# Kernel optimization log

Hardware: AMD Instinct MI355X
Metric: run time of the kernel (lower is better)

## Reference

```python
import jax, jax.numpy as jnp
import numpy as np

D_MODEL = 1024
NUM_HEADS = 16
HEAD_DIM = D_MODEL // NUM_HEADS


def setup_inputs() -> dict:
    key = jax.random.key(0)
    ks = jax.random.split(key, 5)
    x = jax.random.normal(ks[0], (4, 2048, D_MODEL), dtype=jnp.float32)
    # xavier_uniform with gain=0.1 for square (D,D) weights: limit = 0.1*sqrt(6/(D+D))
    limit = 0.1 * np.sqrt(6.0 / (2 * D_MODEL))
    def w(k):
        return jax.random.uniform(k, (D_MODEL, D_MODEL), jnp.float32, -limit, limit)
    return {
        "x": x,
        "W_q": w(ks[1]), "b_q": jnp.zeros((D_MODEL,), jnp.float32),
        "W_k": w(ks[2]), "b_k": jnp.zeros((D_MODEL,), jnp.float32),
        "W_v": w(ks[3]), "b_v": jnp.zeros((D_MODEL,), jnp.float32),
        "W_o": w(ks[4]), "b_o": jnp.zeros((D_MODEL,), jnp.float32),
    }


def reference(x, W_q, b_q, W_k, b_k, W_v, b_v, W_o, b_o):
    B, S, D = x.shape
    H, Hd = NUM_HEADS, HEAD_DIM
    # Linear: x @ W^T + b (torch nn.Linear convention); weights here are (out, in)
    def proj(W, b):
        y = jnp.einsum('bsd,ed->bse', x, W) + b
        return y.reshape(B, S, H, Hd).transpose(0, 2, 1, 3)  # [B,H,S,Hd]
    Q = proj(W_q, b_q)
    K = proj(W_k, b_k)
    V = proj(W_v, b_v)
    scale = 1.0 / np.sqrt(Hd).astype(np.float32)
    scores = jnp.einsum('bhqd,bhkd->bhqk', Q, K) * scale  # [B,H,S,S]
    attn = jax.nn.softmax(scores, axis=-1)
    ctx = jnp.einsum('bhqk,bhkd->bhqd', attn, V)
    ctx = ctx.transpose(0, 2, 1, 3).reshape(B, S, D)
    out = jnp.einsum('bsd,ed->bse', ctx, W_o) + b_o
    return out
```

## Files before the change

### kernel.cpp

```cpp
#include <hip/hip_runtime.h>
#include <math.h>

#define B_  4
#define S_  2048
#define D_  1024
#define H_  16
#define HD_ 64
#define M_  (B_*S_)

typedef short short8 __attribute__((ext_vector_type(8)));
typedef float f32x4 __attribute__((ext_vector_type(4)));

#define MFMA16(a,b,c) __builtin_amdgcn_mfma_f32_16x16x32_bf16(a, b, c, 0, 0, 0)

#if __has_builtin(__builtin_amdgcn_exp2f)
#define EXP2(x) __builtin_amdgcn_exp2f(x)
#else
#define EXP2(x) exp2f(x)
#endif

__device__ __forceinline__ unsigned short f2bf(float f) {
    unsigned u = __float_as_uint(f);
    u = (u + 0x7FFF + ((u >> 16) & 1)) >> 16;
    return (unsigned short)u;
}

__device__ __forceinline__ unsigned pack_bf16(float a, float b) {
#if __has_builtin(__builtin_amdgcn_cvt_pk_bf16_f32)
    typedef __bf16 bf2 __attribute__((ext_vector_type(2)));
    bf2 v = __builtin_amdgcn_cvt_pk_bf16_f32(a, b);
    unsigned r;
    __builtin_memcpy(&r, &v, 4);
    return r;
#else
    unsigned ua = __float_as_uint(a), ub = __float_as_uint(b);
    ua += 0x7FFFu + ((ua >> 16) & 1u);
    ub += 0x7FFFu + ((ub >> 16) & 1u);
    return __builtin_amdgcn_perm(ub, ua, 0x07060302u);
#endif
}

__device__ __forceinline__ void async_copy16(const void* g, void* l) {
    __builtin_amdgcn_global_load_lds(
        (const __attribute__((address_space(1))) void*)g,
        (__attribute__((address_space(3))) void*)l, 16, 0, 0);
}

__global__ __launch_bounds__(256) void cvt_all(
    const float* __restrict__ x,
    const float* __restrict__ w0, const float* __restrict__ w1,
    const float* __restrict__ w2, const float* __restrict__ w3,
    unsigned short* __restrict__ xb, unsigned short* __restrict__ wb)
{
    size_t i = ((size_t)blockIdx.x * 256 + threadIdx.x) * 4;
    const float* src; unsigned short* dst;
    if (i < (size_t)M_ * D_) {
        src = x + i; dst = xb + i;
    } else {
        size_t j = i - (size_t)M_ * D_;
        int z = (int)(j >> 20);
        const float* w = (z == 0) ? w0 : (z == 1) ? w1 : (z == 2) ? w2 : w3;
        src = w + (j & ((size_t)D_ * D_ - 1)); dst = wb + j;
    }
    float4 v = *(const float4*)src;
    uint2 o;
    o.x = pack_bf16(v.x, v.y);
    o.y = pack_bf16(v.z, v.w);
    *(uint2*)dst = o;
}

__device__ __forceinline__ void gemm_body(
    const unsigned short* __restrict__ A, const unsigned short* __restrict__ W,
    const float* __restrict__ bias, void* __restrict__ out,
    int mode, float cscale, int bx, int by)
{
    __shared__ unsigned short As[128 * 64];
    __shared__ unsigned short Ws[128 * 64];
    const int K = D_;
    int tid = threadIdx.x;
    int w = tid >> 6, lane = tid & 63;
    int quad = lane >> 4, l16 = lane & 15;
    int r8 = lane >> 3, c8 = lane & 7;
    int cK = c8 ^ r8;
    int wm = w >> 2, wn = w & 3;
    int m0 = by * 128, n0 = bx * 128;
    int fl = l16 & 7;

    f32x4 acc[4][2];
    #pragma unroll
    for (int i = 0; i < 4; ++i)
        #pragma unroll
        for (int j = 0; j < 2; ++j)
            acc[i][j] = (f32x4){0.f, 0.f, 0.f, 0.f};

    const unsigned short* Ag = A + (size_t)(m0 + w * 8 + r8) * K + cK * 8;
    const unsigned short* Wg = W + (size_t)(n0 + w * 8 + r8) * K + cK * 8;

    for (int k0 = 0; k0 < K; k0 += 64) {
        __syncthreads();
        #pragma unroll
        for (int ii = 0; ii < 2; ++ii) {
            async_copy16(Ag + k0 + (size_t)ii * 64 * K, As + (ii * 64 + w * 8) * 64);
            async_copy16(Wg + k0 + (size_t)ii * 64 * K, Ws + (ii * 64 + w * 8) * 64);
        }
        __syncthreads();
        #pragma unroll
        for (int s = 0; s < 2; ++s) {
            int st = ((quad + s * 4) ^ fl) * 8;
            short8 a[4], b[2];
            #pragma unroll
            for (int i = 0; i < 4; ++i)
                a[i] = *(const short8*)&As[(wm * 64 + i * 16 + l16) * 64 + st];
            #pragma unroll
            for (int j = 0; j < 2; ++j)
                b[j] = *(const short8*)&Ws[(wn * 32 + j * 16 + l16) * 64 + st];
            #pragma unroll
            for (int i = 0; i < 4; ++i)
                #pragma unroll
                for (int j = 0; j < 2; ++j)
                    acc[i][j] = MFMA16(a[i], b[j], acc[i][j]);
        }
    }

    #pragma unroll
    for (int i = 0; i < 4; ++i) {
        int mb = m0 + wm * 64 + i * 16 + quad * 4;
        #pragma unroll
        for (int j = 0; j < 2; ++j) {
            int n = n0 + wn * 32 + j * 16 + l16;
            float bn = bias[n];
            if (mode == 0) {
                #pragma unroll
                for (int r = 0; r < 4; ++r)
                    ((float*)out)[(size_t)(mb + r) * D_ + n] = acc[i][j][r] + bn;
            } else if (mode == 1) {
                int h = n >> 6, hd = n & 63;
                #pragma unroll
                for (int r = 0; r < 4; ++r) {
                    int m = mb + r;
                    int bb = m >> 11, s = m & (S_ - 1);
                    ((unsigned short*)out)[(((size_t)(bb * H_ + h)) * S_ + s) * HD_ + hd] =
                        f2bf((acc[i][j][r] + bn) * cscale);
                }
            } else {
                int h = n >> 6, hd = n & 63;
                int bb = mb >> 11, s0 = mb & (S_ - 1);
                uint2 o;
                o.x = pack_bf16(acc[i][j][0] + bn, acc[i][j][1] + bn);
                o.y = pack_bf16(acc[i][j][2] + bn, acc[i][j][3] + bn);
                *(uint2*)&((unsigned short*)out)[(((size_t)(bb * H_ + h)) * HD_ + hd) * S_ + s0] = o;
            }
        }
    }
}

__global__ __launch_bounds__(512) void qkv_gemm(
    const unsigned short* __restrict__ A,
    const unsigned short* __restrict__ Wq, const unsigned short* __restrict__ Wk,
    const unsigned short* __restrict__ Wv,
    const float* __restrict__ bq, const float* __restrict__ bk, const float* __restrict__ bv,
    unsigned short* Qo, unsigned short* Ko, unsigned short* Vo)
{
    int z = blockIdx.z;
    const unsigned short* W = (z == 0) ? Wq : (z == 1) ? Wk : Wv;
    const float* bias = (z == 0) ? bq : (z == 1) ? bk : bv;
    unsigned short* out = (z == 0) ? Qo : (z == 1) ? Ko : Vo;
    float cscale = (z == 0) ? 0.125f * 1.44269504088896f : 1.0f;
    int mode = (z == 2) ? 2 : 1;
    gemm_body(A, W, bias, out, mode, cscale, blockIdx.x, blockIdx.y);
}

__global__ __launch_bounds__(512) void out_gemm(
    const unsigned short* __restrict__ A, const unsigned short* __restrict__ W,
    const float* __restrict__ bias, float* __restrict__ out)
{
    gemm_body(A, W, bias, out, 0, 1.0f, blockIdx.x, blockIdx.y);
}

__global__ __launch_bounds__(512, 4) void attn_mfma(
    const unsigned short* __restrict__ Q, const unsigned short* __restrict__ K,
    const unsigned short* __restrict__ VT, unsigned short* __restrict__ ctx)
{
    __shared__ unsigned short Ks[2 * 64 * 64];
    __shared__ unsigned short VTs[2 * 64 * 64];
    __shared__ unsigned short QPs[256 * 64];

    int tid = threadIdx.x;
    int w = tid >> 6, lane = tid & 63;
    int quad = lane >> 4, l16 = lane & 15;
    int r8 = lane >> 3, c8 = lane & 7;
    int cK = c8 ^ r8;
    int fl  = l16 & 7;
    int fl2 = (l16 ^ (l16 >> 1)) & 7;
    int bh = blockIdx.x;
    int q0 = blockIdx.y * 256;

    const unsigned short* Qp = Q + ((size_t)bh * S_ + q0) * HD_;
    const unsigned short* Kp = K + (size_t)bh * S_ * HD_;
    const unsigned short* Vp = VT + (size_t)bh * HD_ * S_;

    int cQ = c8 ^ r8 ^ (r8 >> 1) ^ ((w & 1) * 4);
    #pragma unroll
    for (int ii = 0; ii < 4; ++ii)
        async_copy16(Qp + (size_t)(ii * 64 + w * 8 + r8) * HD_ + cQ * 8,
                     QPs + (ii * 64 + w * 8) * 64);
    async_copy16(Kp + (size_t)(w * 8 + r8) * HD_ + cK * 8, Ks + (w * 8) * 64);
    async_copy16(Vp + (size_t)(w * 8 + r8) * S_ + cK * 8, VTs + (w * 8) * 64);
    __syncthreads();

    short8 bq_[2][2];
    #pragma unroll
    for (int mt = 0; mt < 2; ++mt)
        #pragma unroll
        for (int s = 0; s < 2; ++s)
            bq_[mt][s] = *(const short8*)&QPs[(w * 32 + mt * 16 + l16) * 64 +
                                              (((quad + s * 4) ^ fl2) * 8)];

    f32x4 O[2][4];
    float lsum[2] = {0.f, 0.f};
    #pragma unroll
    for (int mt = 0; mt < 2; ++mt)
        #pragma unroll
        for (int nt = 0; nt < 4; ++nt) O[mt][nt] = (f32x4){0.f, 0.f, 0.f, 0.f};

    int cur = 0;
    for (int kt = 0; kt < S_ / 64; ++kt) {
        if (kt + 1 < S_ / 64) {
            int nb = (cur ^ 1) * 4096;
            async_copy16(Kp + (size_t)((kt + 1) * 64 + w * 8 + r8) * HD_ + cK * 8,
                         Ks + nb + (w * 8) * 64);
            async_copy16(Vp + (size_t)(w * 8 + r8) * S_ + (kt + 1) * 64 + cK * 8,
                         VTs + nb + (w * 8) * 64);
        }
        const unsigned short* ks  = Ks + cur * 4096;
        const unsigned short* vts = VTs + cur * 4096;

        f32x4 sc[2][4];
        #pragma unroll
        for (int mt = 0; mt < 2; ++mt)
            #pragma unroll
            for (int nt = 0; nt < 4; ++nt) sc[mt][nt] = (f32x4){0.f, 0.f, 0.f, 0.f};
        #pragma unroll
        for (int s = 0; s < 2; ++s) {
            int stk = ((quad + s * 4) ^ fl) * 8;
            #pragma unroll
            for (int nt = 0; nt < 4; ++nt) {
                short8 ak = *(const short8*)&ks[(nt * 16 + l16) * 64 + stk];
                sc[0][nt] = MFMA16(ak, bq_[0][s], sc[0][nt]);
                sc[1][nt] = MFMA16(ak, bq_[1][s], sc[1][nt]);
            }
        }

        #pragma unroll
        for (int mt = 0; mt < 2; ++mt) {
            #pragma unroll
            for (int nt = 0; nt < 4; ++nt) {
                float p0 = EXP2(sc[mt][nt][0]);
                float p1 = EXP2(sc[mt][nt][1]);
                float p2 = EXP2(sc[mt][nt][2]);
                float p3 = EXP2(sc[mt][nt][3]);
                lsum[mt] += (p0 + p1) + (p2 + p3);
                uint2 pk;
                pk.x = pack_bf16(p0, p1);
                pk.y = pack_bf16(p2, p3);
                int addr = (w * 32 + mt * 16 + l16) * 64 +
                           (((nt * 2 + (quad >> 1)) ^ fl2) * 8) + (quad & 1) * 4;
                *(uint2*)&QPs[addr] = pk;
            }
        }

        #pragma unroll
        for (int s = 0; s < 2; ++s) {
            int stp = ((quad + s * 4) ^ fl2) * 8;
            int stv = ((quad + s * 4) ^ fl) * 8;
            short8 pa0 = *(const short8*)&QPs[(w * 32 + l16) * 64 + stp];
            short8 pa1 = *(const short8*)&QPs[(w * 32 + 16 + l16) * 64 + stp];
            #pragma unroll
            for (int nt = 0; nt < 4; ++nt) {
                short8 bv_ = *(const short8*)&vts[(nt * 16 + l16) * 64 + stv];
                O[0][nt] = MFMA16(pa0, bv_, O[0][nt]);
                O[1][nt] = MFMA16(pa1, bv_, O[1][nt]);
            }
        }

        __syncthreads();
        cur ^= 1;
    }

    float linv[2];
    #pragma unroll
    for (int mt = 0; mt < 2; ++mt) {
        float l = lsum[mt];
        l += __shfl_xor(l, 16);
        l += __shfl_xor(l, 32);
        linv[mt] = 1.0f / l;
    }

    int b = bh >> 4, h = bh & (H_ - 1);
    #pragma unroll
    for (int mt = 0; mt < 2; ++mt)
        #pragma unroll
        for (int r = 0; r < 4; ++r) {
            float inv = __shfl(linv[mt], quad * 4 + r, 64);
            int q = q0 + w * 32 + mt * 16 + quad * 4 + r;
            size_t base = ((size_t)(b * S_) + q) * D_ + h * HD_;
            #pragma unroll
            for (int nt = 0; nt < 4; ++nt)
                ctx[base + nt * 16 + l16] = f2bf(O[mt][nt][r] * inv);
        }
}

extern "C" void kernel_launch(void* const* d_in, const int* in_sizes, int n_in,
                              void* d_out, int out_size, void* d_ws, size_t ws_size,
                              hipStream_t stream) {
    const float* x  = (const float*)d_in[0];
    const float* Wq = (const float*)d_in[1];
    const float* bq = (const float*)d_in[2];
    const float* Wk = (const float*)d_in[3];
    const float* bk = (const float*)d_in[4];
    const float* Wv = (const float*)d_in[5];
    const float* bv = (const float*)d_in[6];
    const float* Wo = (const float*)d_in[7];
    const float* bo = (const float*)d_in[8];

    unsigned short* xb  = (unsigned short*)d_ws;
    unsigned short* wb  = xb + (size_t)M_ * D_;
    unsigned short* Qb  = wb + (size_t)4 * D_ * D_;
    unsigned short* Kb  = Qb + (size_t)M_ * D_;
    unsigned short* VTb = Kb + (size_t)M_ * D_;
    unsigned short* ctb = VTb + (size_t)M_ * D_;

    int cvt_blocks = (M_ * D_ + 4 * D_ * D_) / 1024;
    cvt_all<<<cvt_blocks, 256, 0, stream>>>(x, Wq, Wk, Wv, Wo, xb, wb);

    qkv_gemm<<<dim3(D_ / 128, M_ / 128, 3), 512, 0, stream>>>(
        xb, wb, wb + (size_t)D_ * D_, wb + (size_t)2 * D_ * D_,
        bq, bk, bv, Qb, Kb, VTb);

    attn_mfma<<<dim3(B_ * H_, S_ / 256), 512, 0, stream>>>(Qb, Kb, VTb, ctb);

    out_gemm<<<dim3(D_ / 128, M_ / 128), 512, 0, stream>>>(
        ctb, wb + (size_t)3 * D_ * D_, bo, (float*)d_out);
}
```

Baseline: 286.8 us.

## Replace QKV GEMM with 256x256-tile ping-pong pipelined kernel over fused weights

Replaces the 128x128-tile QKV projection with a new kernel that computes 256x256 output tiles over the concatenated Wq/Wk/Wv matrix. The K loop is double-buffered and split into four phases, with async prefetch of the next A and W tiles interleaved between MFMA blocks, s_setprio raised around the MFMA sections, and explicit barriers between phases. Larger tiles raise arithmetic intensity and cut global and LDS traffic per FLOP, at the cost of 128 KB of LDS per block, heavy register use, and fewer blocks in flight. It also adds setprio hints around the MFMA loops in the attention kernel.

```diff
diff --git a/kernel.cpp b/kernel.cpp
--- a/kernel.cpp
+++ b/kernel.cpp
@@ -67,6 +67,166 @@
     o.x = pack_bf16(v.x, v.y);
     o.y = pack_bf16(v.z, v.w);
     *(uint2*)dst = o;
+}
+
+__global__ __launch_bounds__(512, 2) void qkv8(
+    const unsigned short* __restrict__ A,
+    const unsigned short* __restrict__ W,
+    const float* __restrict__ bq, const float* __restrict__ bk,
+    const float* __restrict__ bv,
+    unsigned short* __restrict__ Qo, unsigned short* __restrict__ Ko,
+    unsigned short* __restrict__ Vo)
+{
+    __shared__ unsigned short As[2][256 * 64];
+    __shared__ unsigned short Ws[2][256 * 64];
+    const int K = D_;
+    int tid = threadIdx.x;
+    int w = tid >> 6, lane = tid & 63;
+    int quad = lane >> 4, l16 = lane & 15;
+    int r8 = lane >> 3, c8 = lane & 7;
+    int cK = c8 ^ r8;
+    int wm = w >> 2, wn = w & 3;
+    int m0 = blockIdx.y * 256, n0 = blockIdx.x * 256;
+    int fl = l16 & 7;
+
+    int z = n0 >> 10;
+    const float* bias = (z == 0) ? bq : (z == 1) ? bk : bv;
+    unsigned short* out = (z == 0) ? Qo : (z == 1) ? Ko : Vo;
+    float cscale = (z == 0) ? 0.125f * 1.44269504088896f : 1.0f;
+
+    f32x4 acc[8][4];
+    #pragma unroll
+    for (int i = 0; i < 8; ++i)
+        #pragma unroll
+        for (int j = 0; j < 4; ++j)
+            acc[i][j] = (f32x4){0.f, 0.f, 0.f, 0.f};
+
+    const unsigned short* Ag = A + (size_t)(m0 + w * 8 + r8) * K + cK * 8;
+    const unsigned short* Wg = W + (size_t)(n0 + w * 8 + r8) * K + cK * 8;
+
+    auto stageA = [&](int slot, int kt) {
+        #pragma unroll
+        for (int ii = 0; ii < 4; ++ii)
+            async_copy16(Ag + (size_t)(ii * 64) * K + kt * 64,
+                         &As[slot][(ii * 64 + w * 8) * 64]);
+    };
+    auto stageW = [&](int slot, int kt) {
+        #pragma unroll
+        for (int ii = 0; ii < 4; ++ii)
+            async_copy16(Wg + (size_t)(ii * 64) * K + kt * 64,
+                         &Ws[slot][(ii * 64 + w * 8) * 64]);
+    };
+
+    stageA(0, 0);
+    stageW(0, 0);
+    __syncthreads();
+
+    #define RDA(cur, i, s) (*(const short8*)&As[cur][(wm * 128 + (i) * 16 + l16) * 64 + \
+                             (((quad + (s) * 4) ^ fl) * 8)])
+    #define RDB(cur, j, s) (*(const short8*)&Ws[cur][(wn * 64 + (j) * 16 + l16) * 64 + \
+                             (((quad + (s) * 4) ^ fl) * 8)])
+
+    for (int kt = 0; kt < 16; ++kt) {
+        int cur = kt & 1;
+        bool pre = (kt < 15);
+        short8 a[4][2], b0[2][2], b1[2][2];
+
+        #pragma unroll
+        for (int i = 0; i < 4; ++i)
+            #pragma unroll
+            for (int s = 0; s < 2; ++s) a[i][s] = RDA(cur, i, s);
+        #pragma unroll
+        for (int j = 0; j < 2; ++j)
+            #pragma unroll
+            for (int s = 0; s < 2; ++s) b0[j][s] = RDB(cur, j, s);
+        if (pre) stageA(cur ^ 1, kt + 1);
+        __builtin_amdgcn_s_setprio(1);
+        #pragma unroll
+        for (int i = 0; i < 4; ++i)
+            #pragma unroll
+            for (int j = 0; j < 2; ++j)
+                #pragma unroll
+                for (int s = 0; s < 2; ++s)
+                    acc[i][j] = MFMA16(a[i][s], b0[j][s], acc[i][j]);
+        __builtin_amdgcn_s_setprio(0);
+        __builtin_amdgcn_s_barrier();
+        __builtin_amdgcn_sched_barrier(0);
+
+        #pragma unroll
+        for (int j = 0; j < 2; ++j)
+            #pragma unroll
+            for (int s = 0; s < 2; ++s) b1[j][s] = RDB(cur, j + 2, s);
+        if (pre) stageW(cur ^ 1, kt + 1);
+        __builtin_amdgcn_s_setprio(1);
+        #pragma unroll
+        for (int i = 0; i < 4; ++i)
+            #pragma unroll
+            for (int j = 0; j < 2; ++j)
+                #pragma unroll
+                for (int s = 0; s < 2; ++s)
+                    acc[i][j + 2] = MFMA16(a[i][s], b1[j][s], acc[i][j + 2]);
+        __builtin_amdgcn_s_setprio(0);
+        __builtin_amdgcn_s_barrier();
+        __builtin_amdgcn_sched_barrier(0);
+
+        #pragma unroll
+        for (int i = 0; i < 4; ++i)
+            #pragma unroll
+            for (int s = 0; s < 2; ++s) a[i][s] = RDA(cur, i + 4, s);
+        __builtin_amdgcn_s_setprio(1);
+        #pragma unroll
+        for (int i = 0; i < 4; ++i)
+            #pragma unroll
+            for (int j = 0; j < 2; ++j)
+                #pragma unroll
+                for (int s = 0; s < 2; ++s)
+                    acc[i + 4][j + 2] = MFMA16(a[i][s], b1[j][s], acc[i + 4][j + 2]);
+        __builtin_amdgcn_s_setprio(0);
+        __builtin_amdgcn_s_barrier();
+        __builtin_amdgcn_sched_barrier(0);
+
+        __builtin_amdgcn_s_setprio(1);
+        #pragma unroll
+        for (int i = 0; i < 4; ++i)
+            #pragma unroll
+            for (int j = 0; j < 2; ++j)
+                #pragma unroll
+                for (int s = 0; s < 2; ++s)
+                    acc[i + 4][j] = MFMA16(a[i][s], b0[j][s], acc[i + 4][j]);
+        __builtin_amdgcn_s_setprio(0);
+        asm volatile("s_waitcnt vmcnt(0)" ::: "memory");
+        __builtin_amdgcn_s_barrier();
+        __builtin_amdgcn_sched_barrier(0);
+    }
+    #undef RDA
+    #undef RDB
+
+    #pragma unroll
+    for (int i = 0; i < 8; ++i) {
+        int mb = m0 + wm * 128 + i * 16 + quad * 4;
+        #pragma unroll
+        for (int j = 0; j < 4; ++j) {
+            int n = n0 + wn * 64 + j * 16 + l16;
+            int nn = n & 1023;
+            float bn = bias[nn];
+            int h = nn >> 6, hd = nn & 63;
+            if (z != 2) {
+                #pragma unroll
+                for (int r = 0; r < 4; ++r) {
+                    int m = mb + r;
+                    int bb = m >> 11, s = m & (S_ - 1);
+                    out[(((size_t)(bb * H_ + h)) * S_ + s) * HD_ + hd] =
+                        f2bf((acc[i][j][r] + bn) * cscale);
+                }
+            } else {
+                int bb = mb >> 11, s0 = mb & (S_ - 1);
+                uint2 o;
+                o.x = pack_bf16(acc[i][j][0] + bn, acc[i][j][1] + bn);
+                o.y = pack_bf16(acc[i][j][2] + bn, acc[i][j][3] + bn);
+                *(uint2*)&out[(((size_t)(bb * H_ + h)) * HD_ + hd) * S_ + s0] = o;
+            }
+        }
+    }
 }
 
 __device__ __forceinline__ void gemm_body(
@@ -154,22 +314,6 @@
     }
 }
 
-__global__ __launch_bounds__(512) void qkv_gemm(
-    const unsigned short* __restrict__ A,
-    const unsigned short* __restrict__ Wq, const unsigned short* __restrict__ Wk,
-    const unsigned short* __restrict__ Wv,
-    const float* __restrict__ bq, const float* __restrict__ bk, const float* __restrict__ bv,
-    unsigned short* Qo, unsigned short* Ko, unsigned short* Vo)
-{
-    int z = blockIdx.z;
-    const unsigned short* W = (z == 0) ? Wq : (z == 1) ? Wk : Wv;
-    const float* bias = (z == 0) ? bq : (z == 1) ? bk : bv;
-    unsigned short* out = (z == 0) ? Qo : (z == 1) ? Ko : Vo;
-    float cscale = (z == 0) ? 0.125f * 1.44269504088896f : 1.0f;
-    int mode = (z == 2) ? 2 : 1;
-    gemm_body(A, W, bias, out, mode, cscale, blockIdx.x, blockIdx.y);
-}
-
 __global__ __launch_bounds__(512) void out_gemm(
     const unsigned short* __restrict__ A, const unsigned short* __restrict__ W,
     const float* __restrict__ bias, float* __restrict__ out)
@@ -240,6 +384,7 @@
         for (int mt = 0; mt < 2; ++mt)
             #pragma unroll
             for (int nt = 0; nt < 4; ++nt) sc[mt][nt] = (f32x4){0.f, 0.f, 0.f, 0.f};
+        __builtin_amdgcn_s_setprio(1);
         #pragma unroll
         for (int s = 0; s < 2; ++s) {
             int stk = ((quad + s * 4) ^ fl) * 8;
@@ -250,6 +395,7 @@
                 sc[1][nt] = MFMA16(ak, bq_[1][s], sc[1][nt]);
             }
         }
+        __builtin_amdgcn_s_setprio(0);
 
         #pragma unroll
         for (int mt = 0; mt < 2; ++mt) {
@@ -269,6 +415,7 @@
             }
         }
 
+        __builtin_amdgcn_s_setprio(1);
         #pragma unroll
         for (int s = 0; s < 2; ++s) {
             int stp = ((quad + s * 4) ^ fl2) * 8;
@@ -282,6 +429,7 @@
                 O[1][nt] = MFMA16(pa1, bv_, O[1][nt]);
             }
         }
+        __builtin_amdgcn_s_setprio(0);
 
         __syncthreads();
         cur ^= 1;
@@ -333,9 +481,8 @@
     int cvt_blocks = (M_ * D_ + 4 * D_ * D_) / 1024;
     cvt_all<<<cvt_blocks, 256, 0, stream>>>(x, Wq, Wk, Wv, Wo, xb, wb);
 
-    qkv_gemm<<<dim3(D_ / 128, M_ / 128, 3), 512, 0, stream>>>(
-        xb, wb, wb + (size_t)D_ * D_, wb + (size_t)2 * D_ * D_,
-        bq, bk, bv, Qb, Kb, VTb);
+    qkv8<<<dim3(3 * D_ / 256, M_ / 256), 512, 0, stream>>>(
+        xb, wb, bq, bk, bv, Qb, Kb, VTb);
 
     attn_mfma<<<dim3(B_ * H_, S_ / 256), 512, 0, stream>>>(Qb, Kb, VTb, ctb);
 
```

Result: faster. 280.3 us (-2.3%).

## Double-buffer GEMM tiles, swizzle block order, triple-buffer attention K/V loads

Applied to the files above, without the earlier changes.

The shared GEMM body now double-buffers its A and W LDS tiles, so the next k-tile's async copies are issued before the current tile's MFMAs and only one barrier per iteration is needed. The QKV and output GEMM grids are flattened and remapped so that neighbouring blocks share tiles for better L2 reuse, and the QKV kernel indexes the concatenated weight buffer directly. The attention kernel moves from two to three K/V buffers and prefetches two tiles ahead, using an explicit vmcnt wait plus barrier in place of __syncthreads. The extra LDS raises per-block shared memory, which may lower occupancy, and the hand-placed waitcnt and barrier depend on the compiler's ordering of memory operations.

```diff
diff --git a/kernel.cpp b/kernel.cpp
--- a/kernel.cpp
+++ b/kernel.cpp
@@ -74,8 +74,8 @@
     const float* __restrict__ bias, void* __restrict__ out,
     int mode, float cscale, int bx, int by)
 {
-    __shared__ unsigned short As[128 * 64];
-    __shared__ unsigned short Ws[128 * 64];
+    __shared__ unsigned short As[2][128 * 64];
+    __shared__ unsigned short Ws[2][128 * 64];
     const int K = D_;
     int tid = threadIdx.x;
     int w = tid >> 6, lane = tid & 63;
@@ -93,33 +93,47 @@
         for (int j = 0; j < 2; ++j)
             acc[i][j] = (f32x4){0.f, 0.f, 0.f, 0.f};
 
-    const unsigned short* Ag = A + (size_t)(m0 + w * 8 + r8) * K + cK * 8;
-    const unsigned short* Wg = W + (size_t)(n0 + w * 8 + r8) * K + cK * 8;
-
-    for (int k0 = 0; k0 < K; k0 += 64) {
-        __syncthreads();
+    const unsigned short* Ag = A + (size_t)(m0 + w * 16 + r8) * K + cK * 8;
+    const unsigned short* Wg = W + (size_t)(n0 + w * 16 + r8) * K + cK * 8;
+
+    auto stage = [&](int slot, int kt) {
         #pragma unroll
         for (int ii = 0; ii < 2; ++ii) {
-            async_copy16(Ag + k0 + (size_t)ii * 64 * K, As + (ii * 64 + w * 8) * 64);
-            async_copy16(Wg + k0 + (size_t)ii * 64 * K, Ws + (ii * 64 + w * 8) * 64);
-        }
-        __syncthreads();
+            async_copy16(Ag + (size_t)(ii * 8) * K + kt * 64,
+                         &As[slot][(w * 16 + ii * 8) * 64]);
+            async_copy16(Wg + (size_t)(ii * 8) * K + kt * 64,
+                         &Ws[slot][(w * 16 + ii * 8) * 64]);
+        }
+    };
+
+    stage(0, 0);
+    __syncthreads();
+
+    const int NT = K / 64;
+    for (int kt = 0; kt < NT; ++kt) {
+        int cur = kt & 1;
+        if (kt + 1 < NT) stage(cur ^ 1, kt + 1);
+
         #pragma unroll
         for (int s = 0; s < 2; ++s) {
             int st = ((quad + s * 4) ^ fl) * 8;
             short8 a[4], b[2];
             #pragma unroll
             for (int i = 0; i < 4; ++i)
-                a[i] = *(const short8*)&As[(wm * 64 + i * 16 + l16) * 64 + st];
+                a[i] = *(const short8*)&As[cur][(wm * 64 + i * 16 + l16) * 64 + st];
             #pragma unroll
             for (int j = 0; j < 2; ++j)
-                b[j] = *(const short8*)&Ws[(wn * 32 + j * 16 + l16) * 64 + st];
+                b[j] = *(const short8*)&Ws[cur][(wn * 32 + j * 16 + l16) * 64 + st];
             #pragma unroll
             for (int i = 0; i < 4; ++i)
                 #pragma unroll
                 for (int j = 0; j < 2; ++j)
                     acc[i][j] = MFMA16(a[i], b[j], acc[i][j]);
         }
+
+        asm volatile("s_waitcnt vmcnt(0)" ::: "memory");
+        __builtin_amdgcn_s_barrier();
+        __builtin_amdgcn_sched_barrier(0);
     }
 
     #pragma unroll
@@ -154,35 +168,39 @@
     }
 }
 
-__global__ __launch_bounds__(512) void qkv_gemm(
-    const unsigned short* __restrict__ A,
-    const unsigned short* __restrict__ Wq, const unsigned short* __restrict__ Wk,
-    const unsigned short* __restrict__ Wv,
-    const float* __restrict__ bq, const float* __restrict__ bk, const float* __restrict__ bv,
-    unsigned short* Qo, unsigned short* Ko, unsigned short* Vo)
-{
-    int z = blockIdx.z;
-    const unsigned short* W = (z == 0) ? Wq : (z == 1) ? Wk : Wv;
+__global__ __launch_bounds__(512, 4) void qkv_gemm(
+    const unsigned short* __restrict__ A, const unsigned short* __restrict__ W,
+    const float* __restrict__ bq, const float* __restrict__ bk,
+    const float* __restrict__ bv,
+    unsigned short* __restrict__ Qo, unsigned short* __restrict__ Ko,
+    unsigned short* __restrict__ Vo)
+{
+    int lin = blockIdx.x + 24 * blockIdx.y;
+    int swz = (lin & 7) * 192 + (lin >> 3);
+    int by = swz / 24, bx = swz % 24;
+    int z = bx >> 3, bxl = bx & 7;
     const float* bias = (z == 0) ? bq : (z == 1) ? bk : bv;
     unsigned short* out = (z == 0) ? Qo : (z == 1) ? Ko : Vo;
     float cscale = (z == 0) ? 0.125f * 1.44269504088896f : 1.0f;
     int mode = (z == 2) ? 2 : 1;
-    gemm_body(A, W, bias, out, mode, cscale, blockIdx.x, blockIdx.y);
-}
-
-__global__ __launch_bounds__(512) void out_gemm(
+    gemm_body(A, W + (size_t)z * D_ * D_, bias, out, mode, cscale, bxl, by);
+}
+
+__global__ __launch_bounds__(512, 4) void out_gemm(
     const unsigned short* __restrict__ A, const unsigned short* __restrict__ W,
     const float* __restrict__ bias, float* __restrict__ out)
 {
-    gemm_body(A, W, bias, out, 0, 1.0f, blockIdx.x, blockIdx.y);
+    int lin = blockIdx.x + 8 * blockIdx.y;
+    int swz = (lin & 7) * 64 + (lin >> 3);
+    gemm_body(A, W, bias, out, 0, 1.0f, swz & 7, swz >> 3);
 }
 
 __global__ __launch_bounds__(512, 4) void attn_mfma(
     const unsigned short* __restrict__ Q, const unsigned short* __restrict__ K,
     const unsigned short* __restrict__ VT, unsigned short* __restrict__ ctx)
 {
-    __shared__ unsigned short Ks[2 * 64 * 64];
-    __shared__ unsigned short VTs[2 * 64 * 64];
+    __shared__ unsigned short Ks[3 * 64 * 64];
+    __shared__ unsigned short VTs[3 * 64 * 64];
     __shared__ unsigned short QPs[256 * 64];
 
     int tid = threadIdx.x;
@@ -204,8 +222,13 @@
     for (int ii = 0; ii < 4; ++ii)
         async_copy16(Qp + (size_t)(ii * 64 + w * 8 + r8) * HD_ + cQ * 8,
                      QPs + (ii * 64 + w * 8) * 64);
-    async_copy16(Kp + (size_t)(w * 8 + r8) * HD_ + cK * 8, Ks + (w * 8) * 64);
-    async_copy16(Vp + (size_t)(w * 8 + r8) * S_ + cK * 8, VTs + (w * 8) * 64);
+    #pragma unroll
+    for (int t = 0; t < 2; ++t) {
+        async_copy16(Kp + (size_t)(t * 64 + w * 8 + r8) * HD_ + cK * 8,
+                     Ks + t * 4096 + (w * 8) * 64);
+        async_copy16(Vp + (size_t)(w * 8 + r8) * S_ + t * 64 + cK * 8,
+                     VTs + t * 4096 + (w * 8) * 64);
+    }
     __syncthreads();
 
     short8 bq_[2][2];
@@ -223,17 +246,17 @@
         #pragma unroll
         for (int nt = 0; nt < 4; ++nt) O[mt][nt] = (f32x4){0.f, 0.f, 0.f, 0.f};
 
-    int cur = 0;
-    for (int kt = 0; kt < S_ / 64; ++kt) {
-        if (kt + 1 < S_ / 64) {
-            int nb = (cur ^ 1) * 4096;
-            async_copy16(Kp + (size_t)((kt + 1) * 64 + w * 8 + r8) * HD_ + cK * 8,
+    const int NT = S_ / 64;
+    for (int kt = 0; kt < NT; ++kt) {
+        if (kt + 2 < NT) {
+            int nb = ((kt + 2) % 3) * 4096;
+            async_copy16(Kp + (size_t)((kt + 2) * 64 + w * 8 + r8) * HD_ + cK * 8,
                          Ks + nb + (w * 8) * 64);
-            async_copy16(Vp + (size_t)(w * 8 + r8) * S_ + (kt + 1) * 64 + cK * 8,
+            async_copy16(Vp + (size_t)(w * 8 + r8) * S_ + (kt + 2) * 64 + cK * 8,
                          VTs + nb + (w * 8) * 64);
         }
-        const unsigned short* ks  = Ks + cur * 4096;
-        const unsigned short* vts = VTs + cur * 4096;
+        const unsigned short* ks  = Ks + (kt % 3) * 4096;
+        const unsigned short* vts = VTs + (kt % 3) * 4096;
 
         f32x4 sc[2][4];
         #pragma unroll
@@ -283,8 +306,10 @@
             }
         }
 
-        __syncthreads();
-        cur ^= 1;
+        if (kt + 2 < NT) asm volatile("s_waitcnt vmcnt(2)" ::: "memory");
+        else             asm volatile("s_waitcnt vmcnt(0)" ::: "memory");
+        __builtin_amdgcn_s_barrier();
+        __builtin_amdgcn_sched_barrier(0);
     }
 
     float linv[2];
@@ -333,9 +358,8 @@
     int cvt_blocks = (M_ * D_ + 4 * D_ * D_) / 1024;
     cvt_all<<<cvt_blocks, 256, 0, stream>>>(x, Wq, Wk, Wv, Wo, xb, wb);
 
-    qkv_gemm<<<dim3(D_ / 128, M_ / 128, 3), 512, 0, stream>>>(
-        xb, wb, wb + (size_t)D_ * D_, wb + (size_t)2 * D_ * D_,
-        bq, bk, bv, Qb, Kb, VTb);
+    qkv_gemm<<<dim3(3 * D_ / 128, M_ / 128), 512, 0, stream>>>(
+        xb, wb, bq, bk, bv, Qb, Kb, VTb);
 
     attn_mfma<<<dim3(B_ * H_, S_ / 256), 512, 0, stream>>>(Qb, Kb, VTb, ctb);
 
```

Result: faster. 267.3 us, median of 2 (-6.8%).
